# Performance work log

Measured on AMD Instinct MI355X. Metric: run time of the kernel, lower is better.

Reference implementation:

```python
import jax, jax.numpy as jnp
import numpy as np

T, B, S = 128, 64, 256
H, E, V = 1024, 512, 32000
PAD_ID = 0

def setup_inputs() -> dict:
    key = jax.random.key(0)
    ks = jax.random.split(key, 12)
    sc = lambda *sh: 1.0 / np.sqrt(sh[-1])
    return {
        'target_ids': jax.random.randint(ks[0], (T, B), 0, V, dtype=jnp.int32),
        'visual_context': jax.random.normal(ks[1], (B, S, 2 * H), jnp.float32),
        'h0': jax.random.normal(ks[2], (B, H), jnp.float32),
        'c0': jax.random.normal(ks[3], (B, H), jnp.float32),
        'E_tgt': jax.random.normal(ks[4], (V, E), jnp.float32) * 0.02,
        'W_att': jax.random.normal(ks[5], (H, 2 * H), jnp.float32) * sc(2 * H),
        'b_att': jnp.zeros((H,), jnp.float32),
        'W_ih': jax.random.normal(ks[6], (4 * H, E + H), jnp.float32) * sc(E + H),
        'W_hh': jax.random.normal(ks[7], (4 * H, H), jnp.float32) * sc(H),
        'W_u': jax.random.normal(ks[8], (H, 3 * H), jnp.float32) * sc(3 * H),
        'W_vocab': jax.random.normal(ks[9], (V, H), jnp.float32) * sc(H),
        'b_vocab': jnp.zeros((V,), jnp.float32),
    }

def reference(target_ids, visual_context, h0, c0, E_tgt, W_att, b_att,
              W_ih, W_hh, W_u, W_vocab, b_vocab):
    # enc_hidden_proj = att_projection(visual_context): (B, S, H)
    enc_proj = jnp.einsum('bsd,hd->bsh', visual_context, W_att) + b_att
    Y = E_tgt[target_ids[:-1]]  # (T-1, B, E) — teacher-forced inputs

    def step(carry, Y_t):
        h, c, o_prev = carry
        Ybar = jnp.concatenate([o_prev, Y_t], axis=1)  # (B, H+E)
        gates = Ybar @ W_ih.T + h @ W_hh.T             # (B, 4H), no bias
        i, f, g, o = jnp.split(gates, 4, axis=1)       # torch LSTMCell order
        i = jax.nn.sigmoid(i); f = jax.nn.sigmoid(f)
        g = jnp.tanh(g); o = jax.nn.sigmoid(o)
        c = f * c + i * g
        h = o * jnp.tanh(c)
        e_t = jnp.einsum('bsh,bh->bs', enc_proj, h)    # attention scores
        alpha = jax.nn.softmax(e_t, axis=1)
        a_t = jnp.einsum('bs,bsd->bd', alpha, visual_context)  # (B, 2H)
        u_t = jnp.concatenate([a_t, h], axis=1)        # (B, 3H)
        o_t = jnp.tanh(u_t @ W_u.T)                    # dropout = identity (eval)
        return (h, c, o_t), o_t

    o_init = jnp.zeros((h0.shape[0], W_u.shape[0]), h0.dtype)
    _, combined = jax.lax.scan(step, (h0, c0, o_init), Y)  # (T-1, B, H)

    logits = jnp.einsum('tbh,vh->tbv', combined, W_vocab) + b_vocab
    P = jax.nn.log_softmax(logits, axis=-1)            # (T-1, B, V)
    gold = target_ids[1:]                              # (T-1, B)
    gold_lp = jnp.take_along_axis(P, gold[..., None].astype(jnp.int32), axis=-1)[..., 0]
    mask = (gold != PAD_ID).astype(P.dtype)
    scores = (gold_lp * mask).sum(axis=0)              # (B,)
    return scores
```

## Files before the change

kernel.cpp:

```cpp
#include <hip/hip_runtime.h>
#include <hip/hip_bf16.h>

#define TSTEPS 127
#define NBLK 256
#define NVB 250
#define MROWS 8128

typedef unsigned short u16;
typedef unsigned int u32;
typedef unsigned long long u64;
typedef _Float16 f16;
typedef __attribute__((ext_vector_type(8))) short bf16x8;
typedef __attribute__((ext_vector_type(8))) _Float16 f16x8;
typedef __attribute__((ext_vector_type(8))) unsigned short u16x8;
typedef __attribute__((ext_vector_type(4))) float f32x4;

__device__ __forceinline__ u16 f2h(float f){ f16 h=(f16)f; u16 r; __builtin_memcpy(&r,&h,2); return r; }
__device__ __forceinline__ float h2f(u16 u){ f16 h; __builtin_memcpy(&h,&u,2); return (float)h; }
__device__ __forceinline__ float us2f(u16 u){ union{float f;u32 i;}v; v.i=(u32)u<<16; return v.f; }
__device__ __forceinline__ u16 f2us(float f){ __hip_bfloat16 h=__float2bfloat16(f); u16 r; __builtin_memcpy(&r,&h,2); return r; }
__device__ __forceinline__ void split2(float x, u16& hi, u16& lo){
  u16 h = f2us(x); lo = f2us(x - us2f(h)); hi = h;
}

__device__ __forceinline__ u64 ldg64(const u64* p){
  return __hip_atomic_load((u64*)p, __ATOMIC_RELAXED, __HIP_MEMORY_SCOPE_AGENT);
}
__device__ __forceinline__ float ldgf(const float* p){
  return __hip_atomic_load((float*)p, __ATOMIC_RELAXED, __HIP_MEMORY_SCOPE_AGENT);
}
__device__ __forceinline__ void stg64(u64* p, u64 v){
  __hip_atomic_store(p, v, __ATOMIC_RELAXED, __HIP_MEMORY_SCOPE_AGENT);
}
__device__ __forceinline__ void stg32(u32* p, u32 v){
  __hip_atomic_store(p, v, __ATOMIC_RELAXED, __HIP_MEMORY_SCOPE_AGENT);
}
__device__ __forceinline__ void stgf(float* p, float v){
  __hip_atomic_store(p, v, __ATOMIC_RELAXED, __HIP_MEMORY_SCOPE_AGENT);
}
__device__ __forceinline__ f16x8 mk8h(u64 a, u64 b){
  union { u64 q[2]; f16x8 v; } u; u.q[0]=a; u.q[1]=b; return u.v;
}

__device__ __forceinline__ void gbar(u32* flags, u32 token){
  asm volatile("s_waitcnt vmcnt(0) lgkmcnt(0)" ::: "memory");
  __syncthreads();
  if (threadIdx.x == 0)
    __hip_atomic_store(&flags[blockIdx.x*32], token, __ATOMIC_RELAXED, __HIP_MEMORY_SCOPE_AGENT);
  if (threadIdx.x < 64){
    const int l = threadIdx.x;
    for (;;){
      bool ok = true;
#pragma unroll
      for (int i=0;i<4;i++)
        ok &= (__hip_atomic_load(&flags[(l*4+i)*32], __ATOMIC_RELAXED, __HIP_MEMORY_SCOPE_AGENT) >= token);
      if (__all(ok)) break;
      __builtin_amdgcn_s_sleep(8);
    }
  }
  __syncthreads();
}

__global__ void p_wcat(const float* __restrict__ Watt, const float* __restrict__ Wu,
                       float* __restrict__ Wcat){
  int idx = blockIdx.x*256 + threadIdx.x;
  int n = idx >> 11, k = idx & 2047;
  Wcat[idx] = (n < 1024) ? Watt[idx] : Wu[(size_t)(n-1024)*3072 + k];
}

__global__ void p_wy(const float* __restrict__ Wih, u16* __restrict__ WYh, u16* __restrict__ WYl){
  int k = blockIdx.x*256 + threadIdx.x;
  int rp = blockIdx.y;
  int j = (rp & 3)*1024 + (rp >> 2);
  float v = Wih[(size_t)j*1536 + 1024 + k];
  u16 hi, lo; split2(v, hi, lo);
  WYh[(size_t)rp*512 + k] = hi; WYl[(size_t)rp*512 + k] = lo;
}

__global__ void p_wuh(const float* __restrict__ Wu, u16* __restrict__ Wh){
  int k = blockIdx.x*256 + threadIdx.x;
  int j = blockIdx.y;
  Wh[(size_t)j*1024 + k] = f2h(Wu[(size_t)j*3072 + 2048 + k]);
}

__global__ void p_y(const int* __restrict__ ids, const float* __restrict__ Etgt,
                    u16* __restrict__ Yh, u16* __restrict__ Yl){
  int e0 = blockIdx.x*256 + threadIdx.x;
  int row = blockIdx.y;
  int id = ids[row];
  float v = Etgt[(size_t)id*512 + e0];
  u16 hi, lo; split2(v, hi, lo);
  Yh[(size_t)row*512 + e0] = hi; Yl[(size_t)row*512 + e0] = lo;
}

__global__ void p_init(const float* __restrict__ h0,
                       u16* __restrict__ hf, u16* __restrict__ of,
                       u32* __restrict__ flags){
  int idx = blockIdx.x*256 + threadIdx.x;
  if (idx < 65536){
    hf[idx] = f2h(h0[idx]);
    of[idx] = 0;
  } else if (idx < 65536 + 8192){
    flags[idx - 65536] = 0;
  }
}

union SharedU {
  struct { u16 a[128*72]; u16 b[128*72]; } st;
  float cc[128*128];
};

__global__ __launch_bounds__(256) void k_gemm32(
    const float* __restrict__ A, const float* __restrict__ Bm,
    const float* __restrict__ bias, u16* __restrict__ ep, u16* __restrict__ vu)
{
  __shared__ SharedU sm;
  const int tid = threadIdx.x;
  const int lane = tid & 63, w = tid >> 6;
  const int wm = w >> 1, wn = w & 1;
  int lw = blockIdx.y * gridDim.x + blockIdx.x;
  int swz = (lw & 7)*256 + (lw >> 3);
  const int n0 = (swz & 15) * 128, m0 = (swz >> 4) * 128;
  f32x4 acc[4][4];
#pragma unroll
  for (int i=0;i<4;i++)
#pragma unroll
    for (int j=0;j<4;j++) acc[i][j] = (f32x4)(0.f);

  for (int k0 = 0; k0 < 2048; k0 += 64) {
    __syncthreads();
#pragma unroll
    for (int i=0;i<8;i++){
      int idx = tid + i*256;
      int r = idx >> 4, c4 = idx & 15;
      float4 va = *(const float4*)(&A[(size_t)(m0+r)*2048 + k0 + c4*4]);
      ushort4 sa; sa.x=f2h(va.x); sa.y=f2h(va.y); sa.z=f2h(va.z); sa.w=f2h(va.w);
      *(ushort4*)(&sm.st.a[r*72 + c4*4]) = sa;
      float4 vb = *(const float4*)(&Bm[(size_t)(n0+r)*2048 + k0 + c4*4]);
      ushort4 sb; sb.x=f2h(vb.x); sb.y=f2h(vb.y); sb.z=f2h(vb.z); sb.w=f2h(vb.w);
      *(ushort4*)(&sm.st.b[r*72 + c4*4]) = sb;
    }
    __syncthreads();
#pragma unroll
    for (int kk = 0; kk < 64; kk += 32) {
      f16x8 af[4], bfr[4];
      int krow = kk + ((lane >> 4) << 3);
#pragma unroll
      for (int m4=0;m4<4;m4++)
        af[m4] = *(const f16x8*)(&sm.st.a[(wm*64 + m4*16 + (lane & 15))*72 + krow]);
#pragma unroll
      for (int n4=0;n4<4;n4++)
        bfr[n4] = *(const f16x8*)(&sm.st.b[(wn*64 + n4*16 + (lane & 15))*72 + krow]);
#pragma unroll
      for (int m4=0;m4<4;m4++)
#pragma unroll
        for (int n4=0;n4<4;n4++)
          acc[m4][n4] = __builtin_amdgcn_mfma_f32_16x16x32_f16(af[m4], bfr[n4], acc[m4][n4], 0,0,0);
    }
  }
  __syncthreads();
#pragma unroll
  for (int m4=0;m4<4;m4++)
#pragma unroll
    for (int n4=0;n4<4;n4++)
#pragma unroll
      for (int i=0;i<4;i++){
        int row = wm*64 + m4*16 + ((lane>>4)<<2) + i;
        int col = wn*64 + n4*16 + (lane&15);
        sm.cc[row*128 + col] = acc[m4][n4][i];
      }
  __syncthreads();
  for (int idx = tid; idx < 128*128; idx += 256) {
    int row = idx >> 7, col = idx & 127;
    int gm = m0 + row, gn = n0 + col;
    float vv = sm.cc[idx];
    if (gn < 1024) { vv += bias[gn]; ep[(size_t)gm*1024 + gn] = f2h(vv); }
    else           { vu[(size_t)gm*1024 + (gn-1024)] = f2h(vv); }
  }
}

__global__ __launch_bounds__(256) void k_gy(
    const u16* __restrict__ Ah, const u16* __restrict__ Al,
    const u16* __restrict__ Bh, const u16* __restrict__ Bl,
    u16* __restrict__ gY)
{
  __shared__ u16 sah[128*40], sal[128*40], sbh[128*40], sbl[128*40];
  const int tid = threadIdx.x;
  const int lane = tid & 63, w = tid >> 6;
  const int wm = w >> 1, wn = w & 1;
  const int l15 = lane & 15, q8 = (lane>>4)*8;
  int lw = blockIdx.y * gridDim.x + blockIdx.x;
  int swz = (lw & 7)*256 + (lw >> 3);
  const int n0 = (swz & 31)*128, m0 = (swz >> 5)*128;
  f32x4 acc[4][4];
#pragma unroll
  for (int i=0;i<4;i++)
#pragma unroll
    for (int j=0;j<4;j++) acc[i][j] = (f32x4)(0.f);

  for (int k0 = 0; k0 < 512; k0 += 32){
    __syncthreads();
#pragma unroll
    for (int i=0;i<8;i++){
      int idx = i*256 + tid;
      int mat = idx >> 9, sub = idx & 511;
      int r = sub >> 2, c8 = (sub & 3)*8;
      const u16* src = (mat==0)?Ah:(mat==1)?Al:(mat==2)?Bh:Bl;
      size_t base = (mat<2 ? (size_t)(m0+r)*512 : (size_t)(n0+r)*512) + k0 + c8;
      u16x8 v = *(const u16x8*)(src + base);
      u16* dst = (mat==0)?sah:(mat==1)?sal:(mat==2)?sbh:sbl;
      *(u16x8*)(&dst[r*40 + c8]) = v;
    }
    __syncthreads();
    bf16x8 ah[4], al2[4], bh[4], bl2[4];
#pragma unroll
    for (int m4=0;m4<4;m4++){
      ah[m4]  = *(const bf16x8*)(&sah[(wm*64+m4*16+l15)*40 + q8]);
      al2[m4] = *(const bf16x8*)(&sal[(wm*64+m4*16+l15)*40 + q8]);
    }
#pragma unroll
    for (int n4=0;n4<4;n4++){
      bh[n4]  = *(const bf16x8*)(&sbh[(wn*64+n4*16+l15)*40 + q8]);
      bl2[n4] = *(const bf16x8*)(&sbl[(wn*64+n4*16+l15)*40 + q8]);
    }
#pragma unroll
    for (int m4=0;m4<4;m4++)
#pragma unroll
      for (int n4=0;n4<4;n4++){
        acc[m4][n4] = __builtin_amdgcn_mfma_f32_16x16x32_bf16(ah[m4],  bh[n4],  acc[m4][n4], 0,0,0);
        acc[m4][n4] = __builtin_amdgcn_mfma_f32_16x16x32_bf16(al2[m4], bh[n4],  acc[m4][n4], 0,0,0);
        acc[m4][n4] = __builtin_amdgcn_mfma_f32_16x16x32_bf16(ah[m4],  bl2[n4], acc[m4][n4], 0,0,0);
      }
  }
#pragma unroll
  for (int m4=0;m4<4;m4++)
#pragma unroll
    for (int n4=0;n4<4;n4++)
#pragma unroll
      for (int i=0;i<4;i++){
        int gm = m0 + wm*64 + m4*16 + ((lane>>4)<<2) + i;
        int gn = n0 + wn*64 + n4*16 + l15;
        gY[(size_t)gm*4096 + gn] = f2h(acc[m4][n4][i]);
      }
}

struct LoopShared {
  u16 wg[32*2048];
  union {
    struct { float psum[2][64][8]; u32 hstage[32][4]; } p1;
    struct { float al[256]; float pared[4][256]; float red[8]; } p3;
  } u;
};

__global__ __launch_bounds__(256, 1) void k_loop(
    const float* __restrict__ Wih, const float* __restrict__ Whh,
    const float* __restrict__ c0g,
    const u16* __restrict__ Wuh16, const u16* __restrict__ gY,
    const u16* __restrict__ ep, const u16* __restrict__ vuu,
    u16* __restrict__ hf, u16* __restrict__ of,
    float* __restrict__ ebuf, float* __restrict__ phB,
    u16* __restrict__ comb, u32* __restrict__ flags)
{
  __shared__ LoopShared sh;
  const int tid = threadIdx.x, blk = blockIdx.x;
  const int lane = tid & 63, w = tid >> 6;
  const int l15 = lane & 15, q = lane >> 4;
  const int jb = blk >> 1, bhalf = blk & 1;
  const int bsub = w & 1, khalf = w >> 1;
  const int b = bhalf*32 + bsub*16 + l15;

  for (int i = tid; i < 32*512; i += 256){
    int r = i >> 9, c4 = i & 511;
    int jp = jb*32 + r;
    int j  = (jp & 3)*1024 + (jp >> 2);
    float4 v = (c4 < 256) ? *(const float4*)(&Wih[(size_t)j*1536 + c4*4])
                          : *(const float4*)(&Whh[(size_t)j*1024 + (c4-256)*4]);
    ushort4 hh; hh.x=f2h(v.x); hh.y=f2h(v.y); hh.z=f2h(v.z); hh.w=f2h(v.w);
    int byteoff = (r*4096 + c4*8) ^ ((r & 7) << 4);
    *(ushort4*)((char*)sh.wg + byteoff) = hh;
  }
  float cReg0 = 0.f, cReg1 = 0.f;
  if (w < 2){
    cReg0 = c0g[(size_t)b*1024 + jb*8 + q];
    cReg1 = c0g[(size_t)b*1024 + jb*8 + 4 + q];
  }
  __syncthreads();
  const char* wgc = (const char*)sh.wg;

  for (int t = 0; t < TSTEPS; ++t){
    const int p = t & 1;
    const u16* hP = hf + p*65536;
    u16* hN = hf + (p^1)*65536;

    {
      float gy0[4], gy1[4];
      if (w < 2){
        const u16* gb = gY + ((size_t)(t*64 + b))*4096 + jb*32 + q*4;
        ushort4 g0 = *(const ushort4*)(gb);
        ushort4 g1 = *(const ushort4*)(gb + 16);
        gy0[0]=h2f(g0.x); gy0[1]=h2f(g0.y); gy0[2]=h2f(g0.z); gy0[3]=h2f(g0.w);
        gy1[0]=h2f(g1.x); gy1[1]=h2f(g1.y); gy1[2]=h2f(g1.z); gy1[3]=h2f(g1.w);
      }
      const u64* xsrc = (khalf ? (const u64*)hP : (const u64*)of) + b*256;
      f32x4 acc0 = (f32x4)(0.f), acc1 = (f32x4)(0.f);
#pragma unroll 4
      for (int kt = 0; kt < 32; ++kt){
        int base = khalf*2048 + kt*64 + q*16;
        int w0 = (l15*4096 + base) ^ ((l15 & 7) << 4);
        f16x8 wf0 = *(const f16x8*)(wgc + w0);
        f16x8 wf1 = *(const f16x8*)(wgc + w0 + 65536);
        const u64* px = xsrc + kt*8 + q*2;
        f16x8 xf = mk8h(ldg64(px), ldg64(px+1));
        acc0 = __builtin_amdgcn_mfma_f32_16x16x32_f16(wf0, xf, acc0, 0,0,0);
        acc1 = __builtin_amdgcn_mfma_f32_16x16x32_f16(wf1, xf, acc1, 0,0,0);
      }
      if (w >= 2){
        float* ps_ = &sh.u.p1.psum[w-2][lane][0];
#pragma unroll
        for (int i=0;i<4;i++){ ps_[i] = acc0[i]; ps_[4+i] = acc1[i]; }
      }
      __syncthreads();
      if (w < 2){
        const float* ps_ = &sh.u.p1.psum[w][lane][0];
        u16 h0b, h1b;
        {
          float gi = acc0[0]+ps_[0]+gy0[0], gf = acc0[1]+ps_[1]+gy0[1];
          float gg = acc0[2]+ps_[2]+gy0[2], go = acc0[3]+ps_[3]+gy0[3];
          gi = 1.f/(1.f+expf(-gi)); gf = 1.f/(1.f+expf(-gf));
          gg = tanhf(gg);           go = 1.f/(1.f+expf(-go));
          float cn = gf*cReg0 + gi*gg; cReg0 = cn;
          h0b = f2h(go*tanhf(cn));
        }
        {
          float gi = acc1[0]+ps_[4]+gy1[0], gf = acc1[1]+ps_[5]+gy1[1];
          float gg = acc1[2]+ps_[6]+gy1[2], go = acc1[3]+ps_[7]+gy1[3];
          gi = 1.f/(1.f+expf(-gi)); gf = 1.f/(1.f+expf(-gf));
          gg = tanhf(gg);           go = 1.f/(1.f+expf(-go));
          float cn = gf*cReg1 + gi*gg; cReg1 = cn;
          h1b = f2h(go*tanhf(cn));
        }
        int bl = bsub*16 + l15;
        u16* hs = (u16*)sh.u.p1.hstage;
        hs[bl*8 + q] = h0b;
        hs[bl*8 + 4 + q] = h1b;
      }
      __syncthreads();
      if (tid < 128){
        int bl = tid >> 2, sub = tid & 3;
        u32 v = sh.u.p1.hstage[bl][sub];
        stg32((u32*)hN + (size_t)(bhalf*32 + bl)*512 + jb*4 + sub, v);
      }
    }
    gbar(flags, (u32)(t*3 + 1));

    if (blk < 16){
      const int jrow = blk*64 + w*16 + l15;
      const u16* wp = Wuh16 + (size_t)jrow*1024;
      f32x4 pacc[4];
#pragma unroll
      for (int i=0;i<4;i++) pacc[i] = (f32x4)(0.f);
#pragma unroll 2
      for (int kt = 0; kt < 32; ++kt){
        f16x8 bfr = *(const f16x8*)(wp + kt*32 + q*8);
#pragma unroll
        for (int m=0;m<4;m++){
          const u64* px = (const u64*)hN + (size_t)(m*16+l15)*256 + kt*8 + q*2;
          f16x8 xf = mk8h(ldg64(px), ldg64(px+1));
          pacc[m] = __builtin_amdgcn_mfma_f32_16x16x32_f16(xf, bfr, pacc[m], 0,0,0);
        }
      }
#pragma unroll
      for (int m=0;m<4;m++)
#pragma unroll
        for (int i=0;i<4;i++){
          int bb = m*16 + q*4 + i;
          stgf(phB + (size_t)bb*1024 + jrow, pacc[m][i]);
        }
    } else {
      for (int u2 = blk - 16; u2 < 256; u2 += 240){
        const int ab = u2 >> 2, sl = u2 & 3;
        float hr[64];
        {
          const u64* hp = (const u64*)hN + (size_t)ab*256 + l15*16;
#pragma unroll
          for (int i=0;i<16;i++){
            union{u64 q_; u16 s[4];} uu; uu.q_ = ldg64(hp + i);
#pragma unroll
            for (int e=0;e<4;e++) hr[i*4+e] = h2f(uu.s[e]);
          }
        }
        const int rbase = sl*64 + w*16;
#pragma unroll
        for (int rg = 0; rg < 4; rg++){
          int s = rbase + rg*4 + q;
          const u16x8* row = (const u16x8*)(ep + ((size_t)(ab*256 + s))*1024 + l15*64);
          float a = 0.f;
#pragma unroll
          for (int j=0;j<8;j++){
            u16x8 v = row[j];
#pragma unroll
            for (int e=0;e<8;e++) a += h2f(v[e]) * hr[j*8+e];
          }
          a += __shfl_xor(a, 1); a += __shfl_xor(a, 2);
          a += __shfl_xor(a, 4); a += __shfl_xor(a, 8);
          if (l15 == 0) stgf(ebuf + ab*256 + s, a);
        }
      }
    }
    gbar(flags, (u32)(t*3 + 2));

    {
      const int ab = blk >> 2, jq = blk & 3;
      float x = ldgf(ebuf + ab*256 + tid);
      float m_ = x;
#pragma unroll
      for (int off=32; off; off>>=1) m_ = fmaxf(m_, __shfl_xor(m_, off));
      if (lane == 0) sh.u.p3.red[w] = m_;
      __syncthreads();
      m_ = fmaxf(fmaxf(sh.u.p3.red[0],sh.u.p3.red[1]), fmaxf(sh.u.p3.red[2],sh.u.p3.red[3]));
      float pv = expf(x - m_);
      float sv = pv;
#pragma unroll
      for (int off=32; off; off>>=1) sv += __shfl_xor(sv, off);
      if (lane == 0) sh.u.p3.red[4+w] = sv;
      __syncthreads();
      float tot = sh.u.p3.red[4]+sh.u.p3.red[5]+sh.u.p3.red[6]+sh.u.p3.red[7];
      sh.u.p3.al[tid] = pv / tot;
      __syncthreads();
      float a0=0.f, a1=0.f, a2=0.f, a3=0.f;
      const u16* vb = vuu + ((size_t)(ab*256) + w*64)*1024 + jq*256 + lane*4;
      for (int s2=0; s2<64; s2++){
        float aa = sh.u.p3.al[w*64 + s2];
        ushort4 v = *(const ushort4*)(vb + (size_t)s2*1024);
        a0 += aa*h2f(v.x); a1 += aa*h2f(v.y); a2 += aa*h2f(v.z); a3 += aa*h2f(v.w);
      }
      float4 o4; o4.x=a0; o4.y=a1; o4.z=a2; o4.w=a3;
      *(float4*)(&sh.u.p3.pared[w][lane*4]) = o4;
      __syncthreads();
      if (tid < 64){
        const int col = tid*4;
        union{u64 q_; u16 s[4];} uo;
        ushort4 cw;
#pragma unroll
        for (int i=0;i<4;i++){
          float pa = sh.u.p3.pared[0][col+i] + sh.u.p3.pared[1][col+i]
                   + sh.u.p3.pared[2][col+i] + sh.u.p3.pared[3][col+i];
          pa += ldgf(phB + (size_t)ab*1024 + jq*256 + col + i);
          u16 ob = f2h(tanhf(pa));
          uo.s[i] = ob; (&cw.x)[i] = ob;
        }
        stg64((u64*)of + (size_t)ab*256 + jq*64 + tid, uo.q_);
        *(ushort4*)(comb + (size_t)(t*64 + ab)*1024 + jq*256 + col) = cw;
      }
    }
    gbar(flags, (u32)(t*3 + 3));
  }
}

__global__ __launch_bounds__(256) void k_gemm16(
    const u16* __restrict__ A, const float* __restrict__ Bm,
    const float* __restrict__ bias,
    float* __restrict__ pm, float* __restrict__ ps,
    float* __restrict__ gl, const int* __restrict__ ids)
{
  __shared__ SharedU sm;
  const int tid = threadIdx.x;
  const int lane = tid & 63, w = tid >> 6;
  const int wm = w >> 1, wn = w & 1;
  int lw = blockIdx.y * 250 + blockIdx.x;
  int swz = (lw & 7)*2000 + (lw >> 3);
  const int n0 = (swz % 250) * 128, m0 = (swz / 250) * 128;
  f32x4 acc[4][4];
#pragma unroll
  for (int i=0;i<4;i++)
#pragma unroll
    for (int j=0;j<4;j++) acc[i][j] = (f32x4)(0.f);

  for (int k0 = 0; k0 < 1024; k0 += 64) {
    __syncthreads();
#pragma unroll
    for (int i=0;i<8;i++){
      int idx = i*256 + tid;
      int half = idx >> 10, id2 = idx & 1023;
      int r = id2 >> 3, c8 = (id2 & 7)*8;
      if (half == 0){
        int gm = m0 + r;
        u16x8 v = {0,0,0,0,0,0,0,0};
        if (gm < MROWS) v = *(const u16x8*)(A + (size_t)gm*1024 + k0 + c8);
        *(u16x8*)(&sm.st.a[r*72 + c8]) = v;
      } else {
        const float* src = Bm + (size_t)(n0 + r)*1024 + k0 + c8;
        float4 a4 = *(const float4*)src;
        float4 b4 = *(const float4*)(src + 4);
        ushort4 ha; ha.x=f2h(a4.x); ha.y=f2h(a4.y); ha.z=f2h(a4.z); ha.w=f2h(a4.w);
        ushort4 hb; hb.x=f2h(b4.x); hb.y=f2h(b4.y); hb.z=f2h(b4.z); hb.w=f2h(b4.w);
        *(ushort4*)(&sm.st.b[r*72 + c8]) = ha;
        *(ushort4*)(&sm.st.b[r*72 + c8 + 4]) = hb;
      }
    }
    __syncthreads();
#pragma unroll
    for (int kk = 0; kk < 64; kk += 32) {
      f16x8 af[4], bfr[4];
      int krow = kk + ((lane >> 4) << 3);
#pragma unroll
      for (int m4=0;m4<4;m4++)
        af[m4] = *(const f16x8*)(&sm.st.a[(wm*64 + m4*16 + (lane & 15))*72 + krow]);
#pragma unroll
      for (int n4=0;n4<4;n4++)
        bfr[n4] = *(const f16x8*)(&sm.st.b[(wn*64 + n4*16 + (lane & 15))*72 + krow]);
#pragma unroll
      for (int m4=0;m4<4;m4++)
#pragma unroll
        for (int n4=0;n4<4;n4++)
          acc[m4][n4] = __builtin_amdgcn_mfma_f32_16x16x32_f16(af[m4], bfr[n4], acc[m4][n4], 0,0,0);
    }
  }
  __syncthreads();
#pragma unroll
  for (int m4=0;m4<4;m4++)
#pragma unroll
    for (int n4=0;n4<4;n4++)
#pragma unroll
      for (int i=0;i<4;i++){
        int row = wm*64 + m4*16 + ((lane>>4)<<2) + i;
        int col = wn*64 + n4*16 + (lane&15);
        sm.cc[row*128 + col] = acc[m4][n4][i];
      }
  __syncthreads();

  if (tid < 128) {
    int row = tid, gm = m0 + row;
    if (gm < MROWS) {
      float mx = -1e30f;
      for (int j=0;j<128;j++){
        int col = (row + j) & 127;
        float x = sm.cc[row*128+col] + bias[n0+col];
        mx = fmaxf(mx, x);
      }
      float sum = 0.f;
      for (int j=0;j<128;j++){
        int col = (row + j) & 127;
        float x = sm.cc[row*128+col] + bias[n0+col];
        sum += expf(x - mx);
      }
      pm[(size_t)gm*NVB + n0/128] = mx;
      ps[(size_t)gm*NVB + n0/128] = sum;
      int g = ids[gm + 64];
      unsigned d = (unsigned)(g - n0);
      if (d < 128u) gl[gm] = sm.cc[row*128 + (int)d] + bias[g];
    }
  }
}

__global__ void k_reduce(const float* __restrict__ pm, const float* __restrict__ ps,
                         const float* __restrict__ gl, const int* __restrict__ ids,
                         float* __restrict__ out)
{
  int b = blockIdx.x, tid = threadIdx.x;
  int lane = tid & 63, w = tid >> 6;
  __shared__ float wacc[4];
  float accum = 0.f;
  for (int t = w; t < TSTEPS; t += 4) {
    int r = t*64 + b;
    const float* pmr = pm + (size_t)r*NVB;
    const float* psr = ps + (size_t)r*NVB;
    float mx = -1e30f;
    for (int p2 = lane; p2 < NVB; p2 += 64) mx = fmaxf(mx, pmr[p2]);
#pragma unroll
    for (int off=32; off; off>>=1) mx = fmaxf(mx, __shfl_xor(mx, off));
    float sm = 0.f;
    for (int p2 = lane; p2 < NVB; p2 += 64) sm += psr[p2] * expf(pmr[p2] - mx);
#pragma unroll
    for (int off=32; off; off>>=1) sm += __shfl_xor(sm, off);
    if (lane == 0) {
      int g = ids[r + 64];
      if (g != 0) accum += gl[r] - (mx + logf(sm));
    }
  }
  if (lane == 0) wacc[w] = accum;
  __syncthreads();
  if (tid == 0) out[b] = wacc[0]+wacc[1]+wacc[2]+wacc[3];
}

extern "C" void kernel_launch(void* const* d_in, const int* in_sizes, int n_in,
                              void* d_out, int out_size, void* d_ws, size_t ws_size,
                              hipStream_t stream)
{
  const int*   ids  = (const int*)d_in[0];
  const float* vc   = (const float*)d_in[1];
  const float* h0   = (const float*)d_in[2];
  const float* c0   = (const float*)d_in[3];
  const float* Etgt = (const float*)d_in[4];
  const float* Watt = (const float*)d_in[5];
  const float* batt = (const float*)d_in[6];
  const float* Wih  = (const float*)d_in[7];
  const float* Whh  = (const float*)d_in[8];
  const float* Wu   = (const float*)d_in[9];
  const float* Wv   = (const float*)d_in[10];
  const float* bv   = (const float*)d_in[11];
  float* out = (float*)d_out;

  char* p = (char*)d_ws;
  auto alloc = [&](size_t bytes)->char* {
    char* r = p; p += (bytes + 255) & ~(size_t)255; return r;
  };
  u32* flags = (u32*)alloc(32768);
  u16* Yh    = (u16*)alloc((size_t)8192*512*2);
  u16* Yl    = (u16*)alloc((size_t)8192*512*2);
  u16* WYh   = (u16*)alloc((size_t)4096*512*2);
  u16* WYl   = (u16*)alloc((size_t)4096*512*2);
  u16* Wuh16 = (u16*)alloc((size_t)1024*1024*2);
  float* Wcat= (float*)alloc((size_t)2048*2048*4);
  u16* ep    = (u16*)alloc((size_t)64*256*1024*2);
  u16* vuu   = (u16*)alloc((size_t)64*256*1024*2);
  u16* comb  = (u16*)alloc((size_t)8192*1024*2);
  u16* gY    = (u16*)alloc((size_t)8192*4096*2);
  u16* hfbuf = (u16*)alloc((size_t)2*65536*2);
  u16* ofbuf = (u16*)alloc(65536*2);
  float* ebuf= (float*)alloc((size_t)64*256*4);
  float* phB = (float*)alloc((size_t)64*1024*4);
  float* pm  = (float*)alloc((size_t)MROWS*NVB*4);
  float* ps  = (float*)alloc((size_t)MROWS*NVB*4);
  float* gl  = (float*)alloc((size_t)MROWS*4);

  p_init<<<288, 256, 0, stream>>>(h0, hfbuf, ofbuf, flags);
  p_wcat<<<(2048*2048)/256, 256, 0, stream>>>(Watt, Wu, Wcat);
  p_wy<<<dim3(2, 4096), 256, 0, stream>>>(Wih, WYh, WYl);
  p_wuh<<<dim3(4, 1024), 256, 0, stream>>>(Wu, Wuh16);
  p_y<<<dim3(2, 8192), 256, 0, stream>>>(ids, Etgt, Yh, Yl);

  k_gemm32<<<dim3(16, 128), 256, 0, stream>>>(vc, Wcat, batt, ep, vuu);
  k_gy<<<dim3(32, 64), 256, 0, stream>>>(Yh, Yl, WYh, WYl, gY);

  k_loop<<<NBLK, 256, 0, stream>>>(Wih, Whh, c0, Wuh16, gY, ep, vuu,
                                   hfbuf, ofbuf, ebuf, phB, comb, flags);

  k_gemm16<<<dim3(NVB, 64), 256, 0, stream>>>(comb, Wv, bv, pm, ps, gl, ids);
  k_reduce<<<64, 256, 0, stream>>>(pm, ps, gl, ids, out);
}
```

Measured before the change: 13.56 ms.

## Keep LSTM gate weights in registers and stage activations in LDS

The LSTM gate phase is repartitioned so each block owns 64 gate rows and 16 batch rows, not 32 rows and 32 batch. The fp16 weight slice now lives in VGPRs (64 f16x8 per lane), and the per-step o/h activations are loaded cooperatively into swizzled LDS instead of each wave issuing atomic global loads inside the MFMA loop. This is meant to cut per-step global-load latency on the serial recurrence. The cost is heavy register pressure and possible spills, plus an extra barrier each step.

```diff
diff --git a/kernel.cpp b/kernel.cpp
--- a/kernel.cpp
+++ b/kernel.cpp
@@ -30,9 +30,6 @@
   return __hip_atomic_load((float*)p, __ATOMIC_RELAXED, __HIP_MEMORY_SCOPE_AGENT);
 }
 __device__ __forceinline__ void stg64(u64* p, u64 v){
-  __hip_atomic_store(p, v, __ATOMIC_RELAXED, __HIP_MEMORY_SCOPE_AGENT);
-}
-__device__ __forceinline__ void stg32(u32* p, u32 v){
   __hip_atomic_store(p, v, __ATOMIC_RELAXED, __HIP_MEMORY_SCOPE_AGENT);
 }
 __device__ __forceinline__ void stgf(float* p, float v){
@@ -244,10 +241,10 @@
       }
 }
 
-struct LoopShared {
-  u16 wg[32*2048];
+struct alignas(16) LoopShared {
+  u16 xs[16*2048];
   union {
-    struct { float psum[2][64][8]; u32 hstage[32][4]; } p1;
+    struct { float psum[2][64][8]; u16 hstage[16][16]; } p1;
     struct { float al[256]; float pared[4][256]; float red[8]; } p3;
   } u;
 };
@@ -265,27 +262,34 @@
   const int tid = threadIdx.x, blk = blockIdx.x;
   const int lane = tid & 63, w = tid >> 6;
   const int l15 = lane & 15, q = lane >> 4;
-  const int jb = blk >> 1, bhalf = blk & 1;
-  const int bsub = w & 1, khalf = w >> 1;
-  const int b = bhalf*32 + bsub*16 + l15;
-
-  for (int i = tid; i < 32*512; i += 256){
-    int r = i >> 9, c4 = i & 511;
-    int jp = jb*32 + r;
+  const int jt = blk >> 2, bg = blk & 3;
+  const int jhalf = w & 1, khalf = w >> 1;
+
+  f16x8 wreg[2][32];
+#pragma unroll
+  for (int rb=0;rb<2;rb++){
+    int jp = jt*64 + jhalf*32 + rb*16 + l15;
     int j  = (jp & 3)*1024 + (jp >> 2);
-    float4 v = (c4 < 256) ? *(const float4*)(&Wih[(size_t)j*1536 + c4*4])
-                          : *(const float4*)(&Whh[(size_t)j*1024 + (c4-256)*4]);
-    ushort4 hh; hh.x=f2h(v.x); hh.y=f2h(v.y); hh.z=f2h(v.z); hh.w=f2h(v.w);
-    int byteoff = (r*4096 + c4*8) ^ ((r & 7) << 4);
-    *(ushort4*)((char*)sh.wg + byteoff) = hh;
-  }
-  float cReg0 = 0.f, cReg1 = 0.f;
+#pragma unroll
+    for (int kt=0;kt<32;kt++){
+      int k = khalf*1024 + kt*32 + q*8;
+      const float* src = (k < 1536) ? &Wih[(size_t)j*1536 + k]
+                                    : &Whh[(size_t)j*1024 + (k-1536)];
+      float4 a4 = *(const float4*)src;
+      float4 b4 = *(const float4*)(src + 4);
+      union { f16x8 v; f16 e[8]; } wv;
+      wv.e[0]=(f16)a4.x; wv.e[1]=(f16)a4.y; wv.e[2]=(f16)a4.z; wv.e[3]=(f16)a4.w;
+      wv.e[4]=(f16)b4.x; wv.e[5]=(f16)b4.y; wv.e[6]=(f16)b4.z; wv.e[7]=(f16)b4.w;
+      wreg[rb][kt] = wv.v;
+    }
+  }
+  float cReg[2] = {0.f, 0.f};
   if (w < 2){
-    cReg0 = c0g[(size_t)b*1024 + jb*8 + q];
-    cReg1 = c0g[(size_t)b*1024 + jb*8 + 4 + q];
-  }
-  __syncthreads();
-  const char* wgc = (const char*)sh.wg;
+#pragma unroll
+    for (int rb=0;rb<2;rb++)
+      cReg[rb] = c0g[(size_t)(bg*16+l15)*1024 + jt*16 + w*8 + rb*4 + q];
+  }
+  __syncthreads();
 
   for (int t = 0; t < TSTEPS; ++t){
     const int p = t & 1;
@@ -293,62 +297,65 @@
     u16* hN = hf + (p^1)*65536;
 
     {
-      float gy0[4], gy1[4];
-      if (w < 2){
-        const u16* gb = gY + ((size_t)(t*64 + b))*4096 + jb*32 + q*4;
-        ushort4 g0 = *(const ushort4*)(gb);
-        ushort4 g1 = *(const ushort4*)(gb + 16);
-        gy0[0]=h2f(g0.x); gy0[1]=h2f(g0.y); gy0[2]=h2f(g0.z); gy0[3]=h2f(g0.w);
-        gy1[0]=h2f(g1.x); gy1[1]=h2f(g1.y); gy1[2]=h2f(g1.z); gy1[3]=h2f(g1.w);
-      }
-      const u64* xsrc = (khalf ? (const u64*)hP : (const u64*)of) + b*256;
+      const u64* osrc = (const u64*)of + (size_t)(bg*16)*256;
+      const u64* hsrc = (const u64*)hP + (size_t)(bg*16)*256;
+#pragma unroll
+      for (int i=0;i<32;i++){
+        const int bl = i >> 1;
+        const int k4 = (i & 1)*256 + tid;
+        u64 v = (i & 1) ? ldg64(hsrc + (size_t)bl*256 + tid)
+                        : ldg64(osrc + (size_t)bl*256 + tid);
+        int dst = (bl*4096 + k4*8) ^ ((bl & 7) << 4);
+        *(u64*)((char*)sh.xs + dst) = v;
+      }
+    }
+    __syncthreads();
+    {
       f32x4 acc0 = (f32x4)(0.f), acc1 = (f32x4)(0.f);
-#pragma unroll 4
-      for (int kt = 0; kt < 32; ++kt){
-        int base = khalf*2048 + kt*64 + q*16;
-        int w0 = (l15*4096 + base) ^ ((l15 & 7) << 4);
-        f16x8 wf0 = *(const f16x8*)(wgc + w0);
-        f16x8 wf1 = *(const f16x8*)(wgc + w0 + 65536);
-        const u64* px = xsrc + kt*8 + q*2;
-        f16x8 xf = mk8h(ldg64(px), ldg64(px+1));
-        acc0 = __builtin_amdgcn_mfma_f32_16x16x32_f16(wf0, xf, acc0, 0,0,0);
-        acc1 = __builtin_amdgcn_mfma_f32_16x16x32_f16(wf1, xf, acc1, 0,0,0);
+#pragma unroll
+      for (int kt=0; kt<32; ++kt){
+        int byteoff = (l15*4096 + khalf*2048 + kt*64 + q*16) ^ ((l15 & 7) << 4);
+        f16x8 xf = *(const f16x8*)((const char*)sh.xs + byteoff);
+        acc0 = __builtin_amdgcn_mfma_f32_16x16x32_f16(wreg[0][kt], xf, acc0, 0,0,0);
+        acc1 = __builtin_amdgcn_mfma_f32_16x16x32_f16(wreg[1][kt], xf, acc1, 0,0,0);
       }
       if (w >= 2){
-        float* ps_ = &sh.u.p1.psum[w-2][lane][0];
+        float* ps_ = &sh.u.p1.psum[jhalf][lane][0];
 #pragma unroll
         for (int i=0;i<4;i++){ ps_[i] = acc0[i]; ps_[4+i] = acc1[i]; }
       }
       __syncthreads();
       if (w < 2){
         const float* ps_ = &sh.u.p1.psum[w][lane][0];
-        u16 h0b, h1b;
+        const int b = bg*16 + l15;
+        const u16* gb = gY + ((size_t)(t*64 + b))*4096 + jt*64 + w*32 + q*4;
+        ushort4 g0 = *(const ushort4*)(gb);
+        ushort4 g1 = *(const ushort4*)(gb + 16);
+        u16 hbits[2];
         {
-          float gi = acc0[0]+ps_[0]+gy0[0], gf = acc0[1]+ps_[1]+gy0[1];
-          float gg = acc0[2]+ps_[2]+gy0[2], go = acc0[3]+ps_[3]+gy0[3];
+          float gi = acc0[0]+ps_[0]+h2f(g0.x), gf = acc0[1]+ps_[1]+h2f(g0.y);
+          float gg = acc0[2]+ps_[2]+h2f(g0.z), go = acc0[3]+ps_[3]+h2f(g0.w);
           gi = 1.f/(1.f+expf(-gi)); gf = 1.f/(1.f+expf(-gf));
           gg = tanhf(gg);           go = 1.f/(1.f+expf(-go));
-          float cn = gf*cReg0 + gi*gg; cReg0 = cn;
-          h0b = f2h(go*tanhf(cn));
+          float cn = gf*cReg[0] + gi*gg; cReg[0] = cn;
+          hbits[0] = f2h(go*tanhf(cn));
         }
         {
-          float gi = acc1[0]+ps_[4]+gy1[0], gf = acc1[1]+ps_[5]+gy1[1];
-          float gg = acc1[2]+ps_[6]+gy1[2], go = acc1[3]+ps_[7]+gy1[3];
+          float gi = acc1[0]+ps_[4]+h2f(g1.x), gf = acc1[1]+ps_[5]+h2f(g1.y);
+          float gg = acc1[2]+ps_[6]+h2f(g1.z), go = acc1[3]+ps_[7]+h2f(g1.w);
           gi = 1.f/(1.f+expf(-gi)); gf = 1.f/(1.f+expf(-gf));
           gg = tanhf(gg);           go = 1.f/(1.f+expf(-go));
-          float cn = gf*cReg1 + gi*gg; cReg1 = cn;
-          h1b = f2h(go*tanhf(cn));
+          float cn = gf*cReg[1] + gi*gg; cReg[1] = cn;
+          hbits[1] = f2h(go*tanhf(cn));
         }
-        int bl = bsub*16 + l15;
-        u16* hs = (u16*)sh.u.p1.hstage;
-        hs[bl*8 + q] = h0b;
-        hs[bl*8 + 4 + q] = h1b;
+        sh.u.p1.hstage[l15][w*8 + q]     = hbits[0];
+        sh.u.p1.hstage[l15][w*8 + 4 + q] = hbits[1];
       }
       __syncthreads();
-      if (tid < 128){
+      if (tid < 64){
         int bl = tid >> 2, sub = tid & 3;
-        u32 v = sh.u.p1.hstage[bl][sub];
-        stg32((u32*)hN + (size_t)(bhalf*32 + bl)*512 + jb*4 + sub, v);
+        u64 v = *(const u64*)&sh.u.p1.hstage[bl][sub*4];
+        stg64((u64*)hN + (size_t)(bg*16 + bl)*256 + jt*4 + sub, v);
       }
     }
     gbar(flags, (u32)(t*3 + 1));
```

Result: slower. 15.13 ms (+11.6%).

## Split LSTM gate K-reduction across block pairs with global partial-sum handoff

Applied to the files above, without the earlier changes.

The recurrent gate GEMM in the persistent loop kernel is repartitioned. Each block now holds 64 gate rows for one K half (either W_ih's o_prev part or W_hh's h part) instead of 32 rows covering both halves. The o_prev-half block writes its partial sums to a global buffer and raises a per-pair flag. The h-half block waits on that flag, adds the partials and gY, and runs the LSTM cell update. This removes the intra-block split across waves and the extra shared-memory reduction, but adds a cross-block flag dependency and global round-trips on every step.

```diff
diff --git a/kernel.cpp b/kernel.cpp
--- a/kernel.cpp
+++ b/kernel.cpp
@@ -32,9 +32,6 @@
 __device__ __forceinline__ void stg64(u64* p, u64 v){
   __hip_atomic_store(p, v, __ATOMIC_RELAXED, __HIP_MEMORY_SCOPE_AGENT);
 }
-__device__ __forceinline__ void stg32(u32* p, u32 v){
-  __hip_atomic_store(p, v, __ATOMIC_RELAXED, __HIP_MEMORY_SCOPE_AGENT);
-}
 __device__ __forceinline__ void stgf(float* p, float v){
   __hip_atomic_store(p, v, __ATOMIC_RELAXED, __HIP_MEMORY_SCOPE_AGENT);
 }
@@ -98,9 +95,10 @@
                        u32* __restrict__ flags){
   int idx = blockIdx.x*256 + threadIdx.x;
   if (idx < 65536){
-    hf[idx] = f2h(h0[idx]);
+    float hv = h0[idx];
+    hf[idx] = f2h(hv);
     of[idx] = 0;
-  } else if (idx < 65536 + 8192){
+  } else if (idx < 65536 + 8448){
     flags[idx - 65536] = 0;
   }
 }
@@ -245,9 +243,9 @@
 }
 
 struct LoopShared {
-  u16 wg[32*2048];
+  u16 wg[64*1024];
   union {
-    struct { float psum[2][64][8]; u32 hstage[32][4]; } p1;
+    struct { u16 hstage[32][16]; } p1;
     struct { float al[256]; float pared[4][256]; float red[8]; } p3;
   } u;
 };
@@ -259,30 +257,30 @@
     const u16* __restrict__ ep, const u16* __restrict__ vuu,
     u16* __restrict__ hf, u16* __restrict__ of,
     float* __restrict__ ebuf, float* __restrict__ phB,
-    u16* __restrict__ comb, u32* __restrict__ flags)
+    u16* __restrict__ comb, float* __restrict__ psum, u32* __restrict__ flags)
 {
   __shared__ LoopShared sh;
   const int tid = threadIdx.x, blk = blockIdx.x;
   const int lane = tid & 63, w = tid >> 6;
   const int l15 = lane & 15, q = lane >> 4;
-  const int jb = blk >> 1, bhalf = blk & 1;
-  const int bsub = w & 1, khalf = w >> 1;
-  const int b = bhalf*32 + bsub*16 + l15;
-
-  for (int i = tid; i < 32*512; i += 256){
-    int r = i >> 9, c4 = i & 511;
-    int jp = jb*32 + r;
+  const int jg = blk >> 2, kh = (blk >> 1) & 1, bh = blk & 1;
+  u32* pflag = flags + 8192;
+
+  for (int i = tid; i < 64*256; i += 256){
+    int r = i >> 8, c4 = i & 255;
+    int jp = jg*64 + r;
     int j  = (jp & 3)*1024 + (jp >> 2);
-    float4 v = (c4 < 256) ? *(const float4*)(&Wih[(size_t)j*1536 + c4*4])
-                          : *(const float4*)(&Whh[(size_t)j*1024 + (c4-256)*4]);
+    float4 v = kh ? *(const float4*)(&Whh[(size_t)j*1024 + c4*4])
+                  : *(const float4*)(&Wih[(size_t)j*1536 + c4*4]);
     ushort4 hh; hh.x=f2h(v.x); hh.y=f2h(v.y); hh.z=f2h(v.z); hh.w=f2h(v.w);
-    int byteoff = (r*4096 + c4*8) ^ ((r & 7) << 4);
+    int byteoff = (r*2048 + c4*8) ^ ((r & 7) << 4);
     *(ushort4*)((char*)sh.wg + byteoff) = hh;
   }
-  float cReg0 = 0.f, cReg1 = 0.f;
-  if (w < 2){
-    cReg0 = c0g[(size_t)b*1024 + jb*8 + q];
-    cReg1 = c0g[(size_t)b*1024 + jb*8 + 4 + q];
+  float cReg[2] = {0.f, 0.f};
+  if (kh){
+#pragma unroll
+    for (int bt=0;bt<2;bt++)
+      cReg[bt] = c0g[(size_t)(bh*32+bt*16+l15)*1024 + jg*16 + w*4 + q];
   }
   __syncthreads();
   const char* wgc = (const char*)sh.wg;
@@ -293,62 +291,65 @@
     u16* hN = hf + (p^1)*65536;
 
     {
-      float gy0[4], gy1[4];
-      if (w < 2){
-        const u16* gb = gY + ((size_t)(t*64 + b))*4096 + jb*32 + q*4;
-        ushort4 g0 = *(const ushort4*)(gb);
-        ushort4 g1 = *(const ushort4*)(gb + 16);
-        gy0[0]=h2f(g0.x); gy0[1]=h2f(g0.y); gy0[2]=h2f(g0.z); gy0[3]=h2f(g0.w);
-        gy1[0]=h2f(g1.x); gy1[1]=h2f(g1.y); gy1[2]=h2f(g1.z); gy1[3]=h2f(g1.w);
-      }
-      const u64* xsrc = (khalf ? (const u64*)hP : (const u64*)of) + b*256;
-      f32x4 acc0 = (f32x4)(0.f), acc1 = (f32x4)(0.f);
+      const u64* xsrc = kh ? (const u64*)hP : (const u64*)of;
+      f32x4 acc[2];
+      acc[0] = (f32x4)(0.f); acc[1] = (f32x4)(0.f);
 #pragma unroll 4
-      for (int kt = 0; kt < 32; ++kt){
-        int base = khalf*2048 + kt*64 + q*16;
-        int w0 = (l15*4096 + base) ^ ((l15 & 7) << 4);
-        f16x8 wf0 = *(const f16x8*)(wgc + w0);
-        f16x8 wf1 = *(const f16x8*)(wgc + w0 + 65536);
-        const u64* px = xsrc + kt*8 + q*2;
-        f16x8 xf = mk8h(ldg64(px), ldg64(px+1));
-        acc0 = __builtin_amdgcn_mfma_f32_16x16x32_f16(wf0, xf, acc0, 0,0,0);
-        acc1 = __builtin_amdgcn_mfma_f32_16x16x32_f16(wf1, xf, acc1, 0,0,0);
-      }
-      if (w >= 2){
-        float* ps_ = &sh.u.p1.psum[w-2][lane][0];
-#pragma unroll
-        for (int i=0;i<4;i++){ ps_[i] = acc0[i]; ps_[4+i] = acc1[i]; }
-      }
-      __syncthreads();
-      if (w < 2){
-        const float* ps_ = &sh.u.p1.psum[w][lane][0];
-        u16 h0b, h1b;
-        {
-          float gi = acc0[0]+ps_[0]+gy0[0], gf = acc0[1]+ps_[1]+gy0[1];
-          float gg = acc0[2]+ps_[2]+gy0[2], go = acc0[3]+ps_[3]+gy0[3];
+      for (int kt=0; kt<32; ++kt){
+        int wb = ((w*16+l15)*2048 + kt*64 + q*16) ^ ((l15 & 7) << 4);
+        f16x8 wf = *(const f16x8*)(wgc + wb);
+        const u64* px0 = xsrc + (size_t)(bh*32 + l15)*256 + kt*8 + q*2;
+        f16x8 xf0 = mk8h(ldg64(px0), ldg64(px0+1));
+        const u64* px1 = px0 + 16*256;
+        f16x8 xf1 = mk8h(ldg64(px1), ldg64(px1+1));
+        acc[0] = __builtin_amdgcn_mfma_f32_16x16x32_f16(wf, xf0, acc[0], 0,0,0);
+        acc[1] = __builtin_amdgcn_mfma_f32_16x16x32_f16(wf, xf1, acc[1], 0,0,0);
+      }
+      if (!kh){
+        float* pb = psum + ((size_t)(jg*2+bh)*32*64);
+#pragma unroll
+        for (int bt=0;bt<2;bt++){
+          union{u64 qq[2]; float f[4];} uu;
+          uu.f[0]=acc[bt][0]; uu.f[1]=acc[bt][1]; uu.f[2]=acc[bt][2]; uu.f[3]=acc[bt][3];
+          u64* pp = (u64*)(pb + (bt*16+l15)*64 + w*16 + q*4);
+          stg64(pp, uu.qq[0]); stg64(pp+1, uu.qq[1]);
+        }
+        asm volatile("s_waitcnt vmcnt(0)" ::: "memory");
+        __syncthreads();
+        if (tid == 0)
+          __hip_atomic_store(&pflag[jg*2+bh], (u32)(t+1), __ATOMIC_RELAXED, __HIP_MEMORY_SCOPE_AGENT);
+      } else {
+        if (tid == 0){
+          while (__hip_atomic_load(&pflag[jg*2+bh], __ATOMIC_RELAXED, __HIP_MEMORY_SCOPE_AGENT) < (u32)(t+1))
+            __builtin_amdgcn_s_sleep(1);
+        }
+        __syncthreads();
+        const float* pb = psum + ((size_t)(jg*2+bh)*32*64);
+#pragma unroll
+        for (int bt=0;bt<2;bt++){
+          const u64* pp = (const u64*)(pb + (bt*16+l15)*64 + w*16 + q*4);
+          union{u64 qq; float f[2];} u0, u1;
+          u0.qq = ldg64(pp); u1.qq = ldg64(pp+1);
+          int b = bh*32 + bt*16 + l15;
+          const u16* gb = gY + ((size_t)(t*64 + b))*4096 + jg*64 + w*16 + q*4;
+          ushort4 g0 = *(const ushort4*)gb;
+          float gi = acc[bt][0] + u0.f[0] + h2f(g0.x);
+          float gf = acc[bt][1] + u0.f[1] + h2f(g0.y);
+          float gg = acc[bt][2] + u1.f[0] + h2f(g0.z);
+          float go = acc[bt][3] + u1.f[1] + h2f(g0.w);
           gi = 1.f/(1.f+expf(-gi)); gf = 1.f/(1.f+expf(-gf));
           gg = tanhf(gg);           go = 1.f/(1.f+expf(-go));
-          float cn = gf*cReg0 + gi*gg; cReg0 = cn;
-          h0b = f2h(go*tanhf(cn));
-        }
-        {
-          float gi = acc1[0]+ps_[4]+gy1[0], gf = acc1[1]+ps_[5]+gy1[1];
-          float gg = acc1[2]+ps_[6]+gy1[2], go = acc1[3]+ps_[7]+gy1[3];
-          gi = 1.f/(1.f+expf(-gi)); gf = 1.f/(1.f+expf(-gf));
-          gg = tanhf(gg);           go = 1.f/(1.f+expf(-go));
-          float cn = gf*cReg1 + gi*gg; cReg1 = cn;
-          h1b = f2h(go*tanhf(cn));
-        }
-        int bl = bsub*16 + l15;
-        u16* hs = (u16*)sh.u.p1.hstage;
-        hs[bl*8 + q] = h0b;
-        hs[bl*8 + 4 + q] = h1b;
-      }
-      __syncthreads();
-      if (tid < 128){
-        int bl = tid >> 2, sub = tid & 3;
-        u32 v = sh.u.p1.hstage[bl][sub];
-        stg32((u32*)hN + (size_t)(bhalf*32 + bl)*512 + jb*4 + sub, v);
+          float cn = gf*cReg[bt] + gi*gg; cReg[bt] = cn;
+          sh.u.p1.hstage[bt*16+l15][w*4+q] = f2h(go*tanhf(cn));
+        }
+        __syncthreads();
+        if (tid < 64){
+          int bloc = tid >> 1, j8 = (tid & 1)*8;
+          u64 v0 = *(const u64*)&sh.u.p1.hstage[bloc][j8];
+          u64 v1 = *(const u64*)&sh.u.p1.hstage[bloc][j8+4];
+          u64* dst = (u64*)hN + (((size_t)(bh*32+bloc)*1024 + jg*16 + j8) >> 2);
+          stg64(dst, v0); stg64(dst+1, v1);
+        }
       }
     }
     gbar(flags, (u32)(t*3 + 1));
@@ -605,7 +606,7 @@
   auto alloc = [&](size_t bytes)->char* {
     char* r = p; p += (bytes + 255) & ~(size_t)255; return r;
   };
-  u32* flags = (u32*)alloc(32768);
+  u32* flags = (u32*)alloc(36864);
   u16* Yh    = (u16*)alloc((size_t)8192*512*2);
   u16* Yl    = (u16*)alloc((size_t)8192*512*2);
   u16* WYh   = (u16*)alloc((size_t)4096*512*2);
@@ -620,11 +621,12 @@
   u16* ofbuf = (u16*)alloc(65536*2);
   float* ebuf= (float*)alloc((size_t)64*256*4);
   float* phB = (float*)alloc((size_t)64*1024*4);
+  float* psum= (float*)alloc((size_t)128*32*64*4);
   float* pm  = (float*)alloc((size_t)MROWS*NVB*4);
   float* ps  = (float*)alloc((size_t)MROWS*NVB*4);
   float* gl  = (float*)alloc((size_t)MROWS*4);
 
-  p_init<<<288, 256, 0, stream>>>(h0, hfbuf, ofbuf, flags);
+  p_init<<<289, 256, 0, stream>>>(h0, hfbuf, ofbuf, flags);
   p_wcat<<<(2048*2048)/256, 256, 0, stream>>>(Watt, Wu, Wcat);
   p_wy<<<dim3(2, 4096), 256, 0, stream>>>(Wih, WYh, WYl);
   p_wuh<<<dim3(4, 1024), 256, 0, stream>>>(Wu, Wuh16);
@@ -634,7 +636,7 @@
   k_gy<<<dim3(32, 64), 256, 0, stream>>>(Yh, Yl, WYh, WYl, gY);
 
   k_loop<<<NBLK, 256, 0, stream>>>(Wih, Whh, c0, Wuh16, gY, ep, vuu,
-                                   hfbuf, ofbuf, ebuf, phB, comb, flags);
+                                   hfbuf, ofbuf, ebuf, phB, comb, psum, flags);
 
   k_gemm16<<<dim3(NVB, 64), 256, 0, stream>>>(comb, Wv, bv, pm, ps, gl, ids);
   k_reduce<<<64, 256, 0, stream>>>(pm, ps, gl, ids, out);
```

Result: slower. 14.38 ms (+6.1%).
